# Optimization experiments

Measured on AMD Instinct MI355X. Metric: run time of the kernel, lower is better.

## Reference

```python
import jax, jax.numpy as jnp
import numpy as np

D, N, K, NC = 768, 128, 25, 3          # d_model, n_spins, K_mc_eval, n_classes
GAMMA, T_MF, DAMPING = 0.25, 25, 0.7   # mean-field Ising constants from config


def _layernorm(x, g, b):
    m = x.mean(-1, keepdims=True)
    v = ((x - m) ** 2).mean(-1, keepdims=True)
    return (x - m) / jnp.sqrt(v + 1e-5) * g + b


def setup_inputs() -> dict:
    key = jax.random.key(0)
    ks = jax.random.split(key, 16)
    B, S = 256, 128
    return {
        'hidden_states': jax.random.normal(ks[0], (B, S, D), jnp.float32),
        'coalitions': (jax.random.uniform(ks[1], (K, N)) < 0.5).astype(jnp.float32),
        'W_v': jax.random.normal(ks[2], (D, D), jnp.float32) * 0.02,
        'scale': jnp.ones((1,), jnp.float32) * 0.1,
        'local_field': jax.random.normal(ks[3], (N,), jnp.float32) * 0.1,
        'J': jax.random.normal(ks[4], (N, N), jnp.float32) * (0.1 / np.sqrt(N)),
        'Wp': jax.random.normal(ks[5], (D, N), jnp.float32) * 0.02,
        'bp': jnp.zeros((N,), jnp.float32),
        'W1': jax.random.normal(ks[6], (N, 256), jnp.float32) * 0.02,
        'b1': jnp.zeros((256,), jnp.float32),
        'g1': jnp.ones((256,), jnp.float32),
        'be1': jnp.zeros((256,), jnp.float32),
        'W2': jax.random.normal(ks[7], (256, 128), jnp.float32) * 0.02,
        'b2': jnp.zeros((128,), jnp.float32),
        'g2': jnp.ones((128,), jnp.float32),
        'be2': jnp.zeros((128,), jnp.float32),
        'W3': jax.random.normal(ks[8], (128, NC), jnp.float32) * 0.02,
        'b3': jnp.zeros((NC,), jnp.float32),
    }


def reference(hidden_states, coalitions, W_v, scale, local_field, J, Wp, bp,
              W1, b1, g1, be1, W2, b2, g2, be2, W3, b3):
    # --- game theory: all K coalition values in one batched pass ----------
    # coalition_value(f, c) = relu(scale * || sum_n c_n f_n W_v ||).
    # Masking then summing is linear in the mask, so contract mask first.
    feats = hidden_states[:, :N, :]                       # [B, N, D]
    cs = jnp.einsum('kn,bnd->bkd', coalitions, feats)     # [B, K, D]
    proj = jnp.einsum('bkd,de->bke', cs, W_v)             # [B, K, D]
    v = jax.nn.relu(jnp.linalg.norm(proj, axis=-1) * scale[0])  # [B, K]
    # Monte-Carlo Shapley: mean(v | spin i in coalition) - mean(v | not in)
    cnt1 = coalitions.sum(0)                              # [N]
    cnt0 = K - cnt1
    sum_w = v @ coalitions                                # [B, N]
    sum_wo = v.sum(1, keepdims=True) - sum_w
    valid = (cnt1 > 0) & (cnt0 > 0)
    shapley = jnp.where(valid,
                        sum_w / jnp.maximum(cnt1, 1.0) - sum_wo / jnp.maximum(cnt0, 1.0),
                        0.0)                              # [B, N]
    # --- mean-field Ising on projected CLS features -----------------------
    pooled = hidden_states[:, 0, :]                       # [B, D] (CLS)
    m0 = jnp.tanh((pooled @ Wp + bp) * 0.1)               # [B, N]
    Jm = J * (1.0 - jnp.eye(N, dtype=J.dtype))            # zero diagonal

    def step(m, _):
        h = local_field + m @ Jm
        new = jnp.tanh(h / GAMMA)
        return DAMPING * new + (1.0 - DAMPING) * m, None

    m, _ = jax.lax.scan(step, m0, None, length=T_MF)
    h_fin = local_field + m @ Jm
    # log(2*cosh(x)) == logaddexp(x, -x), numerically stable
    free_energy = -GAMMA * jnp.sum(jnp.logaddexp(h_fin / GAMMA, -h_fin / GAMMA),
                                   axis=-1, keepdims=True)   # [B, 1]
    # --- classifier head on expected spins --------------------------------
    x = jax.nn.gelu(_layernorm(m @ W1 + b1, g1, be1), approximate=False)
    x = jax.nn.gelu(_layernorm(x @ W2 + b2, g2, be2), approximate=False)
    logits = x @ W3 + b3                                   # [B, NC]
    return logits, free_energy, shapley
```

## Files before the change

### kernel.cpp

```cpp
#include <hip/hip_runtime.h>
#include <math.h>


typedef _Float16 h8 __attribute__((ext_vector_type(8)));
typedef float f4v __attribute__((ext_vector_type(4)));

constexpr int Bq = 256, Dq = 768, Nq = 128, Kq = 25;
constexpr size_t WVT_OFF  = 0;
constexpr size_t CS_OFF   = 1179648;
constexpr size_t PART_OFF = 11010048;
constexpr size_t M0_OFF   = 11112448;

template <int KS>
__device__ __forceinline__ void ldb24(const float* __restrict__ hb2, float* arr) {
  #pragma unroll
  for (int ct = 0; ct < 3; ++ct) {
    const float* hp = hb2 + (size_t)(KS * 32) * 768 + ct * 16;
    #pragma unroll
    for (int j = 0; j < 8; ++j) arr[ct * 8 + j] = hp[(size_t)j * 768];
  }
}

__device__ __forceinline__ void stepk(const float* arr, const h8& a0, const h8& a1,
                                      f4v acc[2][3]) {
  #pragma unroll
  for (int ct = 0; ct < 3; ++ct) {
    h8 bfv;
    #pragma unroll
    for (int j = 0; j < 8; ++j) bfv[j] = (_Float16)arr[ct * 8 + j];
    acc[0][ct] = __builtin_amdgcn_mfma_f32_16x16x32_f16(a0, bfv, acc[0][ct], 0, 0, 0);
    acc[1][ct] = __builtin_amdgcn_mfma_f32_16x16x32_f16(a1, bfv, acc[1][ct], 0, 0, 0);
  }
}

__global__ __launch_bounds__(256, 2) void k1_front(const float* __restrict__ hst,
                                                   const float* __restrict__ coal,
                                                   const float* __restrict__ Wv,
                                                   const float* __restrict__ Wp,
                                                   const float* __restrict__ bp,
                                                   _Float16* __restrict__ wvt,
                                                   _Float16* __restrict__ csf,
                                                   float* __restrict__ m0g) {
  __shared__ float tile[32 * 33];
  __shared__ float part2[256];
  const int t = threadIdx.x;
  const int b = blockIdx.x & 255;
  const int cc = blockIdx.x >> 8;
  const int l = t & 63, w = t >> 6;
  const int colbase = cc * 192;
  const int kb = (l >> 4) * 8;
  const float* hb = hst + (size_t)b * (128 * 768);

  if (blockIdx.x < 576) {
    const int bx = blockIdx.x % 24, by = blockIdx.x / 24;
    const int r = t >> 3, c4 = (t & 7) * 4;
    const float4 v = *reinterpret_cast<const float4*>(Wv + (size_t)(by * 32 + r) * 768 + bx * 32 + c4);
    tile[r * 33 + c4 + 0] = v.x; tile[r * 33 + c4 + 1] = v.y;
    tile[r * 33 + c4 + 2] = v.z; tile[r * 33 + c4 + 3] = v.w;
    __syncthreads();
    _Float16* dp = wvt + (size_t)(bx * 32 + r) * 768 + by * 32 + c4;
    dp[0] = (_Float16)tile[(c4 + 0) * 33 + r];
    dp[1] = (_Float16)tile[(c4 + 1) * 33 + r];
    dp[2] = (_Float16)tile[(c4 + 2) * 33 + r];
    dp[3] = (_Float16)tile[(c4 + 3) * 33 + r];
  }

  h8 afrag[2][4];
  #pragma unroll
  for (int Mt = 0; Mt < 2; ++Mt) {
    const int row = Mt * 16 + (l & 15);
    #pragma unroll
    for (int ks = 0; ks < 4; ++ks) {
      h8 v;
      if (row < 25) {
        const float4 p0 = *reinterpret_cast<const float4*>(coal + row * 128 + ks * 32 + kb);
        const float4 p1 = *reinterpret_cast<const float4*>(coal + row * 128 + ks * 32 + kb + 4);
        v[0] = (_Float16)p0.x; v[1] = (_Float16)p0.y;
        v[2] = (_Float16)p0.z; v[3] = (_Float16)p0.w;
        v[4] = (_Float16)p1.x; v[5] = (_Float16)p1.y;
        v[6] = (_Float16)p1.z; v[7] = (_Float16)p1.w;
      } else {
        #pragma unroll
        for (int j = 0; j < 8; ++j) v[j] = (_Float16)0.f;
      }
      afrag[Mt][ks] = v;
    }
  }

  f4v acc[2][3];
  #pragma unroll
  for (int Mt = 0; Mt < 2; ++Mt)
    #pragma unroll
    for (int ct = 0; ct < 3; ++ct) acc[Mt][ct] = (f4v){0.f, 0.f, 0.f, 0.f};

  const float* hb2 = hb + (size_t)kb * 768 + colbase + w * 48 + (l & 15);
  float ta[24], tb[24];
  ldb24<0>(hb2, ta);
  ldb24<1>(hb2, tb);
  stepk(ta, afrag[0][0], afrag[1][0], acc);
  ldb24<2>(hb2, ta);
  stepk(tb, afrag[0][1], afrag[1][1], acc);
  ldb24<3>(hb2, tb);
  stepk(ta, afrag[0][2], afrag[1][2], acc);
  stepk(tb, afrag[0][3], afrag[1][3], acc);

  #pragma unroll
  for (int Mt = 0; Mt < 2; ++Mt) {
    const int row0 = Mt * 16 + (l >> 4) * 4;
    #pragma unroll
    for (int ct = 0; ct < 3; ++ct) {
      const int col = colbase + (w * 3 + ct) * 16 + (l & 15);
      #pragma unroll
      for (int r = 0; r < 4; ++r) {
        const int rr = row0 + r;
        if (rr < 25)
          csf[((size_t)b * 25 + rr) * 768 + col] = (_Float16)acc[Mt][ct][r];
      }
    }
  }

  if (cc == 0) {
    const int j = t & 127, sg = t >> 7;
    float s = 0.f;
    for (int d = sg * 384; d < sg * 384 + 384; d += 4) {
      const float4 p4 = *reinterpret_cast<const float4*>(hb + d);
      s += p4.x * Wp[(d + 0) * 128 + j] + p4.y * Wp[(d + 1) * 128 + j]
         + p4.z * Wp[(d + 2) * 128 + j] + p4.w * Wp[(d + 3) * 128 + j];
    }
    part2[t] = s;
    __syncthreads();
    if (t < 128) {
      const float a0 = bp[t] + part2[t] + part2[t + 128];
      m0g[b * 128 + t] = tanhf(a0 * 0.1f);
    }
  }
}

__global__ __launch_bounds__(512, 1) void k2_norm(const _Float16* __restrict__ csA,
                                                  const _Float16* __restrict__ wvtB,
                                                  float* __restrict__ part) {
  __shared__ __align__(16) char lds[(128 + 192) * 64];
  char* ldsA = lds;
  char* ldsB = lds + 8192;
  const int tid = threadIdx.x, l = tid & 63, w = tid >> 6;
  const int rg = blockIdx.x >> 2, cc = blockIdx.x & 3;
  const size_t rowbase = (size_t)rg * 128;
  const int colbase = cc * 192;
  const int wm = w & 1, wn = w >> 1;

  const int fch = ((l >> 4) ^ (((l & 15) >> 1) & 3)) * 16;
  const int aoff = (l & 15) * 64 + fch;
  const int boff = (l & 15) * 64 + fch;

  const int srow = tid >> 2, sich = tid & 3;
  const int sch = sich ^ ((srow >> 1) & 3);
  const size_t gA_base = (rowbase + srow) * 768 + sich * 8;
  const size_t gB0_base = (size_t)(colbase + srow) * 768 + sich * 8;
  const size_t gB1_base = (size_t)(colbase + 128 + srow) * 768 + sich * 8;
  char* ldsA_w = ldsA + srow * 64 + sch * 16;
  char* ldsB0_w = ldsB + srow * 64 + sch * 16;
  char* ldsB1_w = ldsB + (128 + srow) * 64 + sch * 16;

  f4v acc[4][3];
  #pragma unroll
  for (int mt = 0; mt < 4; ++mt)
    #pragma unroll
    for (int nt = 0; nt < 3; ++nt) acc[mt][nt] = (f4v){0.f, 0.f, 0.f, 0.f};

  uint4 ra = *reinterpret_cast<const uint4*>(csA + gA_base);
  uint4 rb0 = *reinterpret_cast<const uint4*>(wvtB + gB0_base);
  uint4 rb1 = {0, 0, 0, 0};
  if (tid < 256) rb1 = *reinterpret_cast<const uint4*>(wvtB + gB1_base);

  for (int ks = 0; ks < 24; ++ks) {
    *reinterpret_cast<uint4*>(ldsA_w) = ra;
    *reinterpret_cast<uint4*>(ldsB0_w) = rb0;
    if (tid < 256) *reinterpret_cast<uint4*>(ldsB1_w) = rb1;
    if (ks < 23) {
      ra = *reinterpret_cast<const uint4*>(csA + gA_base + (ks + 1) * 32);
      rb0 = *reinterpret_cast<const uint4*>(wvtB + gB0_base + (ks + 1) * 32);
      if (tid < 256) rb1 = *reinterpret_cast<const uint4*>(wvtB + gB1_base + (ks + 1) * 32);
    }
    __syncthreads();
    h8 af[4];
    #pragma unroll
    for (int mt = 0; mt < 4; ++mt)
      af[mt] = *reinterpret_cast<const h8*>(ldsA + (wm * 4 + mt) * 1024 + aoff);
    #pragma unroll
    for (int nt = 0; nt < 3; ++nt) {
      const h8 bf = *reinterpret_cast<const h8*>(ldsB + (wn * 3 + nt) * 1024 + boff);
      #pragma unroll
      for (int mt = 0; mt < 4; ++mt)
        acc[mt][nt] = __builtin_amdgcn_mfma_f32_16x16x32_f16(af[mt], bf, acc[mt][nt], 0, 0, 0);
    }
    __syncthreads();
  }

  float* redw = reinterpret_cast<float*>(lds);
  #pragma unroll
  for (int mt = 0; mt < 4; ++mt) {
    #pragma unroll
    for (int r = 0; r < 4; ++r) {
      float s = acc[mt][0][r] * acc[mt][0][r] + acc[mt][1][r] * acc[mt][1][r]
              + acc[mt][2][r] * acc[mt][2][r];
      s += __shfl_xor(s, 1); s += __shfl_xor(s, 2);
      s += __shfl_xor(s, 4); s += __shfl_xor(s, 8);
      if ((l & 15) == 0) {
        const int row_local = (wm * 4 + mt) * 16 + (l >> 4) * 4 + r;
        redw[row_local * 4 + wn] = s;
      }
    }
  }
  __syncthreads();
  if (tid < 128) {
    const float tot = redw[tid * 4 + 0] + redw[tid * 4 + 1]
                    + redw[tid * 4 + 2] + redw[tid * 4 + 3];
    part[(size_t)cc * 6400 + rowbase + tid] = tot;
  }
}

__device__ __forceinline__ float bsum4(float v, float* red) {
  #pragma unroll
  for (int o = 32; o > 0; o >>= 1) v += __shfl_down(v, o, 64);
  __syncthreads();
  if ((threadIdx.x & 63) == 0) red[threadIdx.x >> 6] = v;
  __syncthreads();
  return red[0] + red[1] + red[2] + red[3];
}

__global__ __launch_bounds__(256, 1) void k3_back(
    const float* __restrict__ Jg,   const float* __restrict__ lf,
    const float* __restrict__ m0g,  const float* __restrict__ part,
    const float* __restrict__ coal, const float* __restrict__ scale,
    const float* __restrict__ W1, const float* __restrict__ b1,
    const float* __restrict__ g1, const float* __restrict__ be1,
    const float* __restrict__ W2, const float* __restrict__ b2,
    const float* __restrict__ g2, const float* __restrict__ be2,
    const float* __restrict__ W3, const float* __restrict__ b3,
    float* __restrict__ out) {
  __shared__ __align__(16) float m_sh[128];
  __shared__ float pmf[256];
  __shared__ float vsh[32];
  __shared__ __align__(16) float x1[256];
  __shared__ float x2[128];
  __shared__ float red[8];
  const int t = threadIdx.x, b = blockIdx.x;
  const int tn = t & 127, th = t >> 7;

  float Jreg[64];
  #pragma unroll
  for (int i = 0; i < 64; ++i)
    Jreg[i] = Jg[(size_t)(th * 64 + i) * 128 + tn];

  if (t < 25) {
    const float sq = part[b * 25 + t] + part[6400 + b * 25 + t]
                   + part[12800 + b * 25 + t] + part[19200 + b * 25 + t];
    vsh[t] = fmaxf(sqrtf(sq) * scale[0], 0.f);
  }
  __syncthreads();

  if (t < 128) {
    float sw = 0.f, c1 = 0.f, vs = 0.f;
    #pragma unroll
    for (int k = 0; k < 25; ++k) {
      const float c = coal[k * 128 + t];
      const float vk = vsh[k];
      sw += c * vk; vs += vk; c1 += c;
    }
    const float c0 = 25.f - c1;
    float shap = 0.f;
    if (c1 > 0.5f && c0 > 0.5f)
      shap = sw / fmaxf(c1, 1.f) - (vs - sw) / fmaxf(c0, 1.f);
    out[1024 + b * 128 + t] = shap;
  }

  float mloc = 0.f, lfv = 0.f, Jdg = 0.f;
  if (t < 128) {
    mloc = m0g[b * 128 + t];
    m_sh[t] = mloc;
    lfv = lf[t];
    Jdg = Jg[t * 128 + t];
  }
  __syncthreads();

  float hs = 0.f;
  for (int it = 0; it <= 25; ++it) {
    float ps0 = 0.f, ps1 = 0.f, ps2 = 0.f, ps3 = 0.f;
    #pragma unroll
    for (int q = 0; q < 16; ++q) {
      const float4 m4 = *reinterpret_cast<const float4*>(m_sh + th * 64 + q * 4);
      ps0 += Jreg[q * 4 + 0] * m4.x;
      ps1 += Jreg[q * 4 + 1] * m4.y;
      ps2 += Jreg[q * 4 + 2] * m4.z;
      ps3 += Jreg[q * 4 + 3] * m4.w;
    }
    pmf[t] = (ps0 + ps1) + (ps2 + ps3);
    __syncthreads();
    if (it < 25) {
      if (t < 128) {
        const float h = lfv - mloc * Jdg + pmf[t] + pmf[t + 128];
        mloc = 0.7f * tanhf(h * 4.0f) + 0.3f * mloc;
        m_sh[t] = mloc;
      }
      __syncthreads();
    } else {
      if (t < 128) hs = lfv - mloc * Jdg + pmf[t] + pmf[t + 128];
    }
  }

  {
    const float a2 = (t < 128) ? fabsf(hs * 4.0f) : 0.f;
    const float fe = (t < 128) ? (a2 + log1pf(expf(-2.f * a2))) : 0.f;
    const float tot = bsum4(fe, red);
    if (t == 0) out[768 + b] = -0.25f * tot;
  }

  float u = b1[t];
  #pragma unroll 4
  for (int n = 0; n < 128; n += 4) {
    const float4 m4 = *reinterpret_cast<const float4*>(m_sh + n);
    u += m4.x * W1[(n + 0) * 256 + t] + m4.y * W1[(n + 1) * 256 + t]
       + m4.z * W1[(n + 2) * 256 + t] + m4.w * W1[(n + 3) * 256 + t];
  }
  const float mean1 = bsum4(u, red) * (1.f / 256.f);
  const float xm1 = u - mean1;
  const float var1 = bsum4(xm1 * xm1, red) * (1.f / 256.f);
  const float xln1 = xm1 * rsqrtf(var1 + 1e-5f) * g1[t] + be1[t];
  x1[t] = 0.5f * xln1 * (1.f + erff(xln1 * 0.70710678118654752f));
  __syncthreads();

  float u2 = 0.f;
  if (t < 128) {
    u2 = b2[t];
    #pragma unroll 4
    for (int n = 0; n < 256; n += 4) {
      const float4 x4 = *reinterpret_cast<const float4*>(x1 + n);
      u2 += x4.x * W2[(n + 0) * 128 + t] + x4.y * W2[(n + 1) * 128 + t]
          + x4.z * W2[(n + 2) * 128 + t] + x4.w * W2[(n + 3) * 128 + t];
    }
  }
  const float mean2 = bsum4(t < 128 ? u2 : 0.f, red) * (1.f / 128.f);
  const float xm2 = u2 - mean2;
  const float var2 = bsum4(t < 128 ? xm2 * xm2 : 0.f, red) * (1.f / 128.f);
  if (t < 128) {
    const float xln2 = xm2 * rsqrtf(var2 + 1e-5f) * g2[t] + be2[t];
    x2[t] = 0.5f * xln2 * (1.f + erff(xln2 * 0.70710678118654752f));
  }
  __syncthreads();

  if (t < 3) {
    float lg = b3[t];
    #pragma unroll 4
    for (int n = 0; n < 128; ++n) lg += x2[n] * W3[n * 3 + t];
    out[b * 3 + t] = lg;
  }
}

extern "C" void kernel_launch(void* const* d_in, const int* in_sizes, int n_in,
                              void* d_out, int out_size, void* d_ws, size_t ws_size,
                              hipStream_t stream) {
  const float* hst   = (const float*)d_in[0];
  const float* coal  = (const float*)d_in[1];
  const float* Wv    = (const float*)d_in[2];
  const float* scale = (const float*)d_in[3];
  const float* lf    = (const float*)d_in[4];
  const float* Jg    = (const float*)d_in[5];
  const float* Wp    = (const float*)d_in[6];
  const float* bp    = (const float*)d_in[7];
  const float* W1    = (const float*)d_in[8];
  const float* b1    = (const float*)d_in[9];
  const float* g1    = (const float*)d_in[10];
  const float* be1   = (const float*)d_in[11];
  const float* W2    = (const float*)d_in[12];
  const float* b2    = (const float*)d_in[13];
  const float* g2    = (const float*)d_in[14];
  const float* be2   = (const float*)d_in[15];
  const float* W3    = (const float*)d_in[16];
  const float* b3    = (const float*)d_in[17];
  float* out = (float*)d_out;

  char* ws = (char*)d_ws;
  _Float16* wvt = (_Float16*)(ws + WVT_OFF);
  _Float16* csf = (_Float16*)(ws + CS_OFF);
  float* part   = (float*)(ws + PART_OFF);
  float* m0g    = (float*)(ws + M0_OFF);

  hipLaunchKernelGGL(k1_front, dim3(1024), dim3(256), 0, stream,
                     hst, coal, Wv, Wp, bp, wvt, csf, m0g);
  hipLaunchKernelGGL(k2_norm, dim3(200), dim3(512), 0, stream, csf, wvt, part);
  hipLaunchKernelGGL(k3_back, dim3(256), dim3(256), 0, stream,
                     Jg, lf, m0g, part, coal, scale,
                     W1, b1, g1, be1, W2, b2, g2, be2, W3, b3, out);
}
```

Measured before the change: 82.85 us.

## Run Ising/classifier blocks concurrently with norm GEMM in one launch

Merges the coalition-norm GEMM kernel and the mean-field Ising/classifier work into one launch. The first 200 blocks do the GEMM and the remaining 256 blocks run the Ising iterations and MLP head, which depend only on k1 outputs. The small Shapley reduction that needs the GEMM results moves to a separate tiny kernel. The intent is to hide the latency-bound serial Ising loop behind the GEMM. In exchange the Ising blocks now run at 512 threads with half of them idle, and the combined kernel may use more registers.

```diff
diff --git a/kernel.cpp b/kernel.cpp
--- a/kernel.cpp
+++ b/kernel.cpp
@@ -136,89 +136,6 @@
   }
 }
 
-__global__ __launch_bounds__(512, 1) void k2_norm(const _Float16* __restrict__ csA,
-                                                  const _Float16* __restrict__ wvtB,
-                                                  float* __restrict__ part) {
-  __shared__ __align__(16) char lds[(128 + 192) * 64];
-  char* ldsA = lds;
-  char* ldsB = lds + 8192;
-  const int tid = threadIdx.x, l = tid & 63, w = tid >> 6;
-  const int rg = blockIdx.x >> 2, cc = blockIdx.x & 3;
-  const size_t rowbase = (size_t)rg * 128;
-  const int colbase = cc * 192;
-  const int wm = w & 1, wn = w >> 1;
-
-  const int fch = ((l >> 4) ^ (((l & 15) >> 1) & 3)) * 16;
-  const int aoff = (l & 15) * 64 + fch;
-  const int boff = (l & 15) * 64 + fch;
-
-  const int srow = tid >> 2, sich = tid & 3;
-  const int sch = sich ^ ((srow >> 1) & 3);
-  const size_t gA_base = (rowbase + srow) * 768 + sich * 8;
-  const size_t gB0_base = (size_t)(colbase + srow) * 768 + sich * 8;
-  const size_t gB1_base = (size_t)(colbase + 128 + srow) * 768 + sich * 8;
-  char* ldsA_w = ldsA + srow * 64 + sch * 16;
-  char* ldsB0_w = ldsB + srow * 64 + sch * 16;
-  char* ldsB1_w = ldsB + (128 + srow) * 64 + sch * 16;
-
-  f4v acc[4][3];
-  #pragma unroll
-  for (int mt = 0; mt < 4; ++mt)
-    #pragma unroll
-    for (int nt = 0; nt < 3; ++nt) acc[mt][nt] = (f4v){0.f, 0.f, 0.f, 0.f};
-
-  uint4 ra = *reinterpret_cast<const uint4*>(csA + gA_base);
-  uint4 rb0 = *reinterpret_cast<const uint4*>(wvtB + gB0_base);
-  uint4 rb1 = {0, 0, 0, 0};
-  if (tid < 256) rb1 = *reinterpret_cast<const uint4*>(wvtB + gB1_base);
-
-  for (int ks = 0; ks < 24; ++ks) {
-    *reinterpret_cast<uint4*>(ldsA_w) = ra;
-    *reinterpret_cast<uint4*>(ldsB0_w) = rb0;
-    if (tid < 256) *reinterpret_cast<uint4*>(ldsB1_w) = rb1;
-    if (ks < 23) {
-      ra = *reinterpret_cast<const uint4*>(csA + gA_base + (ks + 1) * 32);
-      rb0 = *reinterpret_cast<const uint4*>(wvtB + gB0_base + (ks + 1) * 32);
-      if (tid < 256) rb1 = *reinterpret_cast<const uint4*>(wvtB + gB1_base + (ks + 1) * 32);
-    }
-    __syncthreads();
-    h8 af[4];
-    #pragma unroll
-    for (int mt = 0; mt < 4; ++mt)
-      af[mt] = *reinterpret_cast<const h8*>(ldsA + (wm * 4 + mt) * 1024 + aoff);
-    #pragma unroll
-    for (int nt = 0; nt < 3; ++nt) {
-      const h8 bf = *reinterpret_cast<const h8*>(ldsB + (wn * 3 + nt) * 1024 + boff);
-      #pragma unroll
-      for (int mt = 0; mt < 4; ++mt)
-        acc[mt][nt] = __builtin_amdgcn_mfma_f32_16x16x32_f16(af[mt], bf, acc[mt][nt], 0, 0, 0);
-    }
-    __syncthreads();
-  }
-
-  float* redw = reinterpret_cast<float*>(lds);
-  #pragma unroll
-  for (int mt = 0; mt < 4; ++mt) {
-    #pragma unroll
-    for (int r = 0; r < 4; ++r) {
-      float s = acc[mt][0][r] * acc[mt][0][r] + acc[mt][1][r] * acc[mt][1][r]
-              + acc[mt][2][r] * acc[mt][2][r];
-      s += __shfl_xor(s, 1); s += __shfl_xor(s, 2);
-      s += __shfl_xor(s, 4); s += __shfl_xor(s, 8);
-      if ((l & 15) == 0) {
-        const int row_local = (wm * 4 + mt) * 16 + (l >> 4) * 4 + r;
-        redw[row_local * 4 + wn] = s;
-      }
-    }
-  }
-  __syncthreads();
-  if (tid < 128) {
-    const float tot = redw[tid * 4 + 0] + redw[tid * 4 + 1]
-                    + redw[tid * 4 + 2] + redw[tid * 4 + 3];
-    part[(size_t)cc * 6400 + rowbase + tid] = tot;
-  }
-}
-
 __device__ __forceinline__ float bsum4(float v, float* red) {
   #pragma unroll
   for (int o = 32; o > 0; o >>= 1) v += __shfl_down(v, o, 64);
@@ -228,132 +145,229 @@
   return red[0] + red[1] + red[2] + red[3];
 }
 
-__global__ __launch_bounds__(256, 1) void k3_back(
+__global__ __launch_bounds__(512, 1) void k23(
+    const _Float16* __restrict__ csA, const _Float16* __restrict__ wvtB,
+    float* __restrict__ part,
     const float* __restrict__ Jg,   const float* __restrict__ lf,
-    const float* __restrict__ m0g,  const float* __restrict__ part,
-    const float* __restrict__ coal, const float* __restrict__ scale,
+    const float* __restrict__ m0g,
     const float* __restrict__ W1, const float* __restrict__ b1,
     const float* __restrict__ g1, const float* __restrict__ be1,
     const float* __restrict__ W2, const float* __restrict__ b2,
     const float* __restrict__ g2, const float* __restrict__ be2,
     const float* __restrict__ W3, const float* __restrict__ b3,
     float* __restrict__ out) {
+  __shared__ __align__(16) char lds[(128 + 192) * 64];
   __shared__ __align__(16) float m_sh[128];
   __shared__ float pmf[256];
-  __shared__ float vsh[32];
   __shared__ __align__(16) float x1[256];
   __shared__ float x2[128];
   __shared__ float red[8];
+  const int tid = threadIdx.x;
+
+  if (blockIdx.x < 200) {
+    char* ldsA = lds;
+    char* ldsB = lds + 8192;
+    const int l = tid & 63, w = tid >> 6;
+    const int rg = blockIdx.x >> 2, cc = blockIdx.x & 3;
+    const size_t rowbase = (size_t)rg * 128;
+    const int colbase = cc * 192;
+    const int wm = w & 1, wn = w >> 1;
+
+    const int fch = ((l >> 4) ^ (((l & 15) >> 1) & 3)) * 16;
+    const int aoff = (l & 15) * 64 + fch;
+    const int boff = (l & 15) * 64 + fch;
+
+    const int srow = tid >> 2, sich = tid & 3;
+    const int sch = sich ^ ((srow >> 1) & 3);
+    const size_t gA_base = (rowbase + srow) * 768 + sich * 8;
+    const size_t gB0_base = (size_t)(colbase + srow) * 768 + sich * 8;
+    const size_t gB1_base = (size_t)(colbase + 128 + srow) * 768 + sich * 8;
+    char* ldsA_w = ldsA + srow * 64 + sch * 16;
+    char* ldsB0_w = ldsB + srow * 64 + sch * 16;
+    char* ldsB1_w = ldsB + (128 + srow) * 64 + sch * 16;
+
+    f4v acc[4][3];
+    #pragma unroll
+    for (int mt = 0; mt < 4; ++mt)
+      #pragma unroll
+      for (int nt = 0; nt < 3; ++nt) acc[mt][nt] = (f4v){0.f, 0.f, 0.f, 0.f};
+
+    uint4 ra = *reinterpret_cast<const uint4*>(csA + gA_base);
+    uint4 rb0 = *reinterpret_cast<const uint4*>(wvtB + gB0_base);
+    uint4 rb1 = {0, 0, 0, 0};
+    if (tid < 256) rb1 = *reinterpret_cast<const uint4*>(wvtB + gB1_base);
+
+    for (int ks = 0; ks < 24; ++ks) {
+      *reinterpret_cast<uint4*>(ldsA_w) = ra;
+      *reinterpret_cast<uint4*>(ldsB0_w) = rb0;
+      if (tid < 256) *reinterpret_cast<uint4*>(ldsB1_w) = rb1;
+      if (ks < 23) {
+        ra = *reinterpret_cast<const uint4*>(csA + gA_base + (ks + 1) * 32);
+        rb0 = *reinterpret_cast<const uint4*>(wvtB + gB0_base + (ks + 1) * 32);
+        if (tid < 256) rb1 = *reinterpret_cast<const uint4*>(wvtB + gB1_base + (ks + 1) * 32);
+      }
+      __syncthreads();
+      h8 af[4];
+      #pragma unroll
+      for (int mt = 0; mt < 4; ++mt)
+        af[mt] = *reinterpret_cast<const h8*>(ldsA + (wm * 4 + mt) * 1024 + aoff);
+      #pragma unroll
+      for (int nt = 0; nt < 3; ++nt) {
+        const h8 bf = *reinterpret_cast<const h8*>(ldsB + (wn * 3 + nt) * 1024 + boff);
+        #pragma unroll
+        for (int mt = 0; mt < 4; ++mt)
+          acc[mt][nt] = __builtin_amdgcn_mfma_f32_16x16x32_f16(af[mt], bf, acc[mt][nt], 0, 0, 0);
+      }
+      __syncthreads();
+    }
+
+    float* redw = reinterpret_cast<float*>(lds);
+    #pragma unroll
+    for (int mt = 0; mt < 4; ++mt) {
+      #pragma unroll
+      for (int r = 0; r < 4; ++r) {
+        float s = acc[mt][0][r] * acc[mt][0][r] + acc[mt][1][r] * acc[mt][1][r]
+                + acc[mt][2][r] * acc[mt][2][r];
+        s += __shfl_xor(s, 1); s += __shfl_xor(s, 2);
+        s += __shfl_xor(s, 4); s += __shfl_xor(s, 8);
+        if ((l & 15) == 0) {
+          const int row_local = (wm * 4 + mt) * 16 + (l >> 4) * 4 + r;
+          redw[row_local * 4 + wn] = s;
+        }
+      }
+    }
+    __syncthreads();
+    if (tid < 128) {
+      const float tot = redw[tid * 4 + 0] + redw[tid * 4 + 1]
+                      + redw[tid * 4 + 2] + redw[tid * 4 + 3];
+      part[(size_t)cc * 6400 + rowbase + tid] = tot;
+    }
+  } else {
+    const int t = tid;
+    const int b = blockIdx.x - 200;
+    const int tn = t & 127, th = t >> 7;
+
+    float Jreg[64];
+    if (t < 256) {
+      #pragma unroll
+      for (int i = 0; i < 64; ++i)
+        Jreg[i] = Jg[(size_t)(th * 64 + i) * 128 + tn];
+    }
+
+    float mloc = 0.f, lfv = 0.f, Jdg = 0.f;
+    if (t < 128) {
+      mloc = m0g[b * 128 + t];
+      m_sh[t] = mloc;
+      lfv = lf[t];
+      Jdg = Jg[t * 128 + t];
+    }
+    __syncthreads();
+
+    float hs = 0.f;
+    for (int it = 0; it <= 25; ++it) {
+      if (t < 256) {
+        float ps0 = 0.f, ps1 = 0.f, ps2 = 0.f, ps3 = 0.f;
+        #pragma unroll
+        for (int q = 0; q < 16; ++q) {
+          const float4 m4 = *reinterpret_cast<const float4*>(m_sh + th * 64 + q * 4);
+          ps0 += Jreg[q * 4 + 0] * m4.x;
+          ps1 += Jreg[q * 4 + 1] * m4.y;
+          ps2 += Jreg[q * 4 + 2] * m4.z;
+          ps3 += Jreg[q * 4 + 3] * m4.w;
+        }
+        pmf[t] = (ps0 + ps1) + (ps2 + ps3);
+      }
+      __syncthreads();
+      if (it < 25) {
+        if (t < 128) {
+          const float h = lfv - mloc * Jdg + pmf[t] + pmf[t + 128];
+          mloc = 0.7f * tanhf(h * 4.0f) + 0.3f * mloc;
+          m_sh[t] = mloc;
+        }
+        __syncthreads();
+      } else {
+        if (t < 128) hs = lfv - mloc * Jdg + pmf[t] + pmf[t + 128];
+      }
+    }
+
+    {
+      const float a2 = (t < 128) ? fabsf(hs * 4.0f) : 0.f;
+      const float fe = (t < 128) ? (a2 + log1pf(expf(-2.f * a2))) : 0.f;
+      const float tot = bsum4(fe, red);
+      if (t == 0) out[768 + b] = -0.25f * tot;
+    }
+
+    float u = 0.f;
+    if (t < 256) {
+      u = b1[t];
+      #pragma unroll 4
+      for (int n = 0; n < 128; n += 4) {
+        const float4 m4 = *reinterpret_cast<const float4*>(m_sh + n);
+        u += m4.x * W1[(n + 0) * 256 + t] + m4.y * W1[(n + 1) * 256 + t]
+           + m4.z * W1[(n + 2) * 256 + t] + m4.w * W1[(n + 3) * 256 + t];
+      }
+    }
+    const float mean1 = bsum4(t < 256 ? u : 0.f, red) * (1.f / 256.f);
+    const float xm1 = u - mean1;
+    const float var1 = bsum4(t < 256 ? xm1 * xm1 : 0.f, red) * (1.f / 256.f);
+    if (t < 256) {
+      const float xln1 = xm1 * rsqrtf(var1 + 1e-5f) * g1[t] + be1[t];
+      x1[t] = 0.5f * xln1 * (1.f + erff(xln1 * 0.70710678118654752f));
+    }
+    __syncthreads();
+
+    float u2 = 0.f;
+    if (t < 128) {
+      u2 = b2[t];
+      #pragma unroll 4
+      for (int n = 0; n < 256; n += 4) {
+        const float4 x4 = *reinterpret_cast<const float4*>(x1 + n);
+        u2 += x4.x * W2[(n + 0) * 128 + t] + x4.y * W2[(n + 1) * 128 + t]
+            + x4.z * W2[(n + 2) * 128 + t] + x4.w * W2[(n + 3) * 128 + t];
+      }
+    }
+    const float mean2 = bsum4(t < 128 ? u2 : 0.f, red) * (1.f / 128.f);
+    const float xm2 = u2 - mean2;
+    const float var2 = bsum4(t < 128 ? xm2 * xm2 : 0.f, red) * (1.f / 128.f);
+    if (t < 128) {
+      const float xln2 = xm2 * rsqrtf(var2 + 1e-5f) * g2[t] + be2[t];
+      x2[t] = 0.5f * xln2 * (1.f + erff(xln2 * 0.70710678118654752f));
+    }
+    __syncthreads();
+
+    if (t < 3) {
+      float lg = b3[t];
+      #pragma unroll 4
+      for (int n = 0; n < 128; ++n) lg += x2[n] * W3[n * 3 + t];
+      out[b * 3 + t] = lg;
+    }
+  }
+}
+
+__global__ __launch_bounds__(128, 1) void k3b(const float* __restrict__ part,
+                                              const float* __restrict__ coal,
+                                              const float* __restrict__ scale,
+                                              float* __restrict__ out) {
+  __shared__ float vsh[32];
   const int t = threadIdx.x, b = blockIdx.x;
-  const int tn = t & 127, th = t >> 7;
-
-  float Jreg[64];
-  #pragma unroll
-  for (int i = 0; i < 64; ++i)
-    Jreg[i] = Jg[(size_t)(th * 64 + i) * 128 + tn];
-
   if (t < 25) {
     const float sq = part[b * 25 + t] + part[6400 + b * 25 + t]
                    + part[12800 + b * 25 + t] + part[19200 + b * 25 + t];
     vsh[t] = fmaxf(sqrtf(sq) * scale[0], 0.f);
   }
   __syncthreads();
-
-  if (t < 128) {
-    float sw = 0.f, c1 = 0.f, vs = 0.f;
-    #pragma unroll
-    for (int k = 0; k < 25; ++k) {
-      const float c = coal[k * 128 + t];
-      const float vk = vsh[k];
-      sw += c * vk; vs += vk; c1 += c;
-    }
-    const float c0 = 25.f - c1;
-    float shap = 0.f;
-    if (c1 > 0.5f && c0 > 0.5f)
-      shap = sw / fmaxf(c1, 1.f) - (vs - sw) / fmaxf(c0, 1.f);
-    out[1024 + b * 128 + t] = shap;
-  }
-
-  float mloc = 0.f, lfv = 0.f, Jdg = 0.f;
-  if (t < 128) {
-    mloc = m0g[b * 128 + t];
-    m_sh[t] = mloc;
-    lfv = lf[t];
-    Jdg = Jg[t * 128 + t];
-  }
-  __syncthreads();
-
-  float hs = 0.f;
-  for (int it = 0; it <= 25; ++it) {
-    float ps0 = 0.f, ps1 = 0.f, ps2 = 0.f, ps3 = 0.f;
-    #pragma unroll
-    for (int q = 0; q < 16; ++q) {
-      const float4 m4 = *reinterpret_cast<const float4*>(m_sh + th * 64 + q * 4);
-      ps0 += Jreg[q * 4 + 0] * m4.x;
-      ps1 += Jreg[q * 4 + 1] * m4.y;
-      ps2 += Jreg[q * 4 + 2] * m4.z;
-      ps3 += Jreg[q * 4 + 3] * m4.w;
-    }
-    pmf[t] = (ps0 + ps1) + (ps2 + ps3);
-    __syncthreads();
-    if (it < 25) {
-      if (t < 128) {
-        const float h = lfv - mloc * Jdg + pmf[t] + pmf[t + 128];
-        mloc = 0.7f * tanhf(h * 4.0f) + 0.3f * mloc;
-        m_sh[t] = mloc;
-      }
-      __syncthreads();
-    } else {
-      if (t < 128) hs = lfv - mloc * Jdg + pmf[t] + pmf[t + 128];
-    }
-  }
-
-  {
-    const float a2 = (t < 128) ? fabsf(hs * 4.0f) : 0.f;
-    const float fe = (t < 128) ? (a2 + log1pf(expf(-2.f * a2))) : 0.f;
-    const float tot = bsum4(fe, red);
-    if (t == 0) out[768 + b] = -0.25f * tot;
-  }
-
-  float u = b1[t];
-  #pragma unroll 4
-  for (int n = 0; n < 128; n += 4) {
-    const float4 m4 = *reinterpret_cast<const float4*>(m_sh + n);
-    u += m4.x * W1[(n + 0) * 256 + t] + m4.y * W1[(n + 1) * 256 + t]
-       + m4.z * W1[(n + 2) * 256 + t] + m4.w * W1[(n + 3) * 256 + t];
-  }
-  const float mean1 = bsum4(u, red) * (1.f / 256.f);
-  const float xm1 = u - mean1;
-  const float var1 = bsum4(xm1 * xm1, red) * (1.f / 256.f);
-  const float xln1 = xm1 * rsqrtf(var1 + 1e-5f) * g1[t] + be1[t];
-  x1[t] = 0.5f * xln1 * (1.f + erff(xln1 * 0.70710678118654752f));
-  __syncthreads();
-
-  float u2 = 0.f;
-  if (t < 128) {
-    u2 = b2[t];
-    #pragma unroll 4
-    for (int n = 0; n < 256; n += 4) {
-      const float4 x4 = *reinterpret_cast<const float4*>(x1 + n);
-      u2 += x4.x * W2[(n + 0) * 128 + t] + x4.y * W2[(n + 1) * 128 + t]
-          + x4.z * W2[(n + 2) * 128 + t] + x4.w * W2[(n + 3) * 128 + t];
-    }
-  }
-  const float mean2 = bsum4(t < 128 ? u2 : 0.f, red) * (1.f / 128.f);
-  const float xm2 = u2 - mean2;
-  const float var2 = bsum4(t < 128 ? xm2 * xm2 : 0.f, red) * (1.f / 128.f);
-  if (t < 128) {
-    const float xln2 = xm2 * rsqrtf(var2 + 1e-5f) * g2[t] + be2[t];
-    x2[t] = 0.5f * xln2 * (1.f + erff(xln2 * 0.70710678118654752f));
-  }
-  __syncthreads();
-
-  if (t < 3) {
-    float lg = b3[t];
-    #pragma unroll 4
-    for (int n = 0; n < 128; ++n) lg += x2[n] * W3[n * 3 + t];
-    out[b * 3 + t] = lg;
-  }
+  float sw = 0.f, c1 = 0.f, vs = 0.f;
+  #pragma unroll
+  for (int k = 0; k < 25; ++k) {
+    const float c = coal[k * 128 + t];
+    const float vk = vsh[k];
+    sw += c * vk; vs += vk; c1 += c;
+  }
+  const float c0 = 25.f - c1;
+  float shap = 0.f;
+  if (c1 > 0.5f && c0 > 0.5f)
+    shap = sw / fmaxf(c1, 1.f) - (vs - sw) / fmaxf(c0, 1.f);
+  out[1024 + b * 128 + t] = shap;
 }
 
 extern "C" void kernel_launch(void* const* d_in, const int* in_sizes, int n_in,
@@ -387,8 +401,9 @@
 
   hipLaunchKernelGGL(k1_front, dim3(1024), dim3(256), 0, stream,
                      hst, coal, Wv, Wp, bp, wvt, csf, m0g);
-  hipLaunchKernelGGL(k2_norm, dim3(200), dim3(512), 0, stream, csf, wvt, part);
-  hipLaunchKernelGGL(k3_back, dim3(256), dim3(256), 0, stream,
-                     Jg, lf, m0g, part, coal, scale,
+  hipLaunchKernelGGL(k23, dim3(456), dim3(512), 0, stream,
+                     csf, wvt, part, Jg, lf, m0g,
                      W1, b1, g1, be1, W2, b2, g2, be2, W3, b3, out);
-}
+  hipLaunchKernelGGL(k3b, dim3(256), dim3(128), 0, stream,
+                     part, coal, scale, out);
+}
```

New measurement: 69.20 us. -16.5%, faster.
